# Kernel optimization log

Hardware: AMD Instinct MI355X
Metric: run time of the kernel (lower is better)

The kernel has to match this reference:

```python
import jax, jax.numpy as jnp
import numpy as np

G1 = 8      # channel groups
G2 = 16     # spatial blocks per side
C1, C2 = 128, 64
H1 = W1 = 128
H2 = W2 = 256
BS1 = H1 // G2   # 8  -> 64 elems per x1 block
BS2 = H2 // G2   # 16 -> 256 elems per x2 block
BN_EPS = 1e-5


def setup_inputs() -> dict:
    key = jax.random.key(0)
    ks = jax.random.split(key, 16)
    B = 4
    c1g, c2g = C1 // G1, C2 // G1          # 16, 8
    inp = {
        "x1": jax.random.normal(ks[0], (B, C1, H1, W1), jnp.float32),
        "x2": jax.random.normal(ks[1], (B, C2, H2, W2), jnp.float32),
        # Conv1: conv1d k=1, C1//G1 -> C1//2//G1  (16 -> 8)
        "w_c1": jax.random.normal(ks[2], (c1g // 2, c1g), jnp.float32) * 0.1,
        "b_c1": jnp.zeros((c1g // 2,), jnp.float32),
        # Conv2: conv1d k=1, C2//G1 -> C2//G1  (8 -> 8)
        "w_c2": jax.random.normal(ks[3], (c2g, c2g), jnp.float32) * 0.1,
        "b_c2": jnp.zeros((c2g,), jnp.float32),
        # conv1 / conv2: 1x1 conv2d to 1 channel
        "w_p1": jax.random.normal(ks[4], (C1,), jnp.float32) * 0.1,
        "b_p1": jnp.zeros((), jnp.float32),
        "w_p2": jax.random.normal(ks[5], (C2,), jnp.float32) * 0.1,
        "b_p2": jnp.zeros((), jnp.float32),
        # SpatialAttention linear: 64 -> 256 (torch weight layout [out, in])
        "w_lin": jax.random.normal(ks[6], (BS2 * BS2, BS1 * BS1), jnp.float32) * 0.1,
        "b_lin": jnp.zeros((BS2 * BS2,), jnp.float32),
        # convbnrelu: 1x1 conv C2->C2 + BN (eval mode, running stats mean=0 var=1)
        "w_f": jax.random.normal(ks[7], (C2, C2), jnp.float32) * 0.05,
        "b_f": jnp.zeros((C2,), jnp.float32),
        "bn_gamma": jnp.ones((C2,), jnp.float32),
        "bn_beta": jnp.zeros((C2,), jnp.float32),
    }
    return inp


def reference(x1, x2, w_c1, b_c1, w_c2, b_c2, w_p1, b_p1, w_p2, b_p2,
              w_lin, b_lin, w_f, b_f, bn_gamma, bn_beta):
    B = x1.shape[0]
    c1g, c2g = C1 // G1, C2 // G1

    # ---- grouped channel attention (vectorized over the 8 groups) ----
    gap1 = x1.reshape(B, G1, c1g, H1 * W1).mean(-1)           # [B,g,16]
    gap2 = x2.reshape(B, G1, c2g, H2 * W2).mean(-1)           # [B,g,8]
    mlp1 = jax.nn.relu(jnp.einsum('oc,bgc->bgo', w_c1, gap1) + b_c1)  # [B,g,8]
    mlp2 = jax.nn.relu(jnp.einsum('oc,bgc->bgo', w_c2, gap2) + b_c2)  # [B,g,8]
    sem = jnp.einsum('bgo,bgp->bgop', mlp1, mlp2)             # [B,g,8,8]
    cw_logits = jnp.einsum('bgop,bgp->bgo', sem, mlp2)        # [B,g,8]
    cw = jax.nn.softmax(cw_logits, axis=-1)                   # softmax over channel dim
    sem_x2 = (x2.reshape(B, G1, c2g, H2, W2) * cw[..., None, None]
              ).reshape(B, C2, H2, W2)

    # ---- block-wise spatial attention (vectorized over 16x16 blocks) ----
    nb = G2 * G2
    x1b = x1.reshape(B, C1, G2, BS1, G2, BS1).transpose(0, 2, 4, 1, 3, 5)
    x1b = x1b.reshape(B, nb, C1, BS1, BS1)
    x2b = x2.reshape(B, C2, G2, BS2, G2, BS2).transpose(0, 2, 4, 1, 3, 5)
    x2b = x2b.reshape(B, nb, C2, BS2, BS2)

    pos1 = (jnp.einsum('c,bncij->bnij', w_p1, x1b) + b_p1).reshape(B, nb, BS1 * BS1)
    pos2 = (jnp.einsum('c,bncij->bnij', w_p2, x2b) + b_p2).reshape(B, nb, BS2 * BS2)

    x1t = jnp.einsum('oc,bnc->bno', w_lin, pos1) + b_lin      # [B,nb,256]
    # bmm(x2^T, x1t) is an outer product since both are rank-1 per block
    scores = pos2[..., :, None] * x1t[..., None, :]           # [B,nb,256,256]
    aw = jax.nn.softmax(scores, axis=-1)
    weighted = jnp.einsum('bnq,bnqk->bnk', pos2, aw)          # [B,nb,256]
    # torch.cat(dim=2).view(B,1,H2,W2): raw row-major flatten of block outputs
    spa = weighted.reshape(B, 1, H2, W2)

    # ---- fuse: 1x1 conv + BN(eval) + ReLU ----
    pre = sem_x2 + spa
    conv = jnp.einsum('oc,bchw->bohw', w_f, pre) + b_f[:, None, None]
    bn = conv / jnp.sqrt(jnp.float32(1.0 + BN_EPS)) * bn_gamma[:, None, None] \
         + bn_beta[:, None, None]
    return jax.nn.relu(bn)
```

## Files before the change

### kernel.cpp

```cpp
#include <hip/hip_runtime.h>


#define GAP_OFF  0
#define POS1_OFF 768
#define POS2_OFF 66304

__global__ __launch_bounds__(256) void k_fuse(const float* __restrict__ x1,
                                              const float* __restrict__ x2,
                                              const float* __restrict__ w_p1,
                                              const float* __restrict__ b_p1,
                                              const float* __restrict__ w_p2,
                                              const float* __restrict__ b_p2,
                                              float* __restrict__ ws) {
  __shared__ float gbuf[128 * 65];
  __shared__ float pbuf[1024];
  int blk = blockIdx.x, t = threadIdx.x;
  int wv = t >> 6, ln = t & 63;
  if (blk < 256) {
    int b = blk >> 6;
    int px0 = (blk & 63) << 8;
    const float* xb = x1 + ((size_t)b << 21) + px0 + (ln << 2);
    float4 pacc; pacc.x = pacc.y = pacc.z = pacc.w = 0.f;
    float gs[32];
#pragma unroll
    for (int i = 0; i < 32; ++i) {
      int c = (i << 2) + wv;
      float4 v = *(const float4*)(xb + ((size_t)c << 14));
      float wc = w_p1[c];
      pacc.x = fmaf(wc, v.x, pacc.x); pacc.y = fmaf(wc, v.y, pacc.y);
      pacc.z = fmaf(wc, v.z, pacc.z); pacc.w = fmaf(wc, v.w, pacc.w);
      gs[i] = (v.x + v.y) + (v.z + v.w);
    }
#pragma unroll
    for (int i = 0; i < 32; ++i) gbuf[((wv << 5) + i) * 65 + ln] = gs[i];
    *(float4*)&pbuf[(wv << 8) + (ln << 2)] = pacc;
    __syncthreads();
    if (t < 128) {
      int w2 = t >> 5, i2 = t & 31;
      int c = (i2 << 2) + w2;
      const float* gp = &gbuf[t * 65];
      float s0 = 0.f, s1 = 0.f, s2 = 0.f, s3 = 0.f;
#pragma unroll
      for (int k = 0; k < 64; k += 4) { s0 += gp[k]; s1 += gp[k+1]; s2 += gp[k+2]; s3 += gp[k+3]; }
      atomicAdd(&ws[GAP_OFF + b * 128 + c], (s0 + s1) + (s2 + s3));
    }
    float s = (pbuf[t] + pbuf[256 + t]) + (pbuf[512 + t] + pbuf[768 + t]) + b_p1[0];
    int p = px0 + t, h = p >> 7, w0 = p & 127;
    int n = ((h >> 3) << 4) + (w0 >> 3);
    ws[POS1_OFF + ((b * 256 + n) << 6) + ((h & 7) << 3) + (w0 & 7)] = s;
  } else {
    int j = blk - 256;
    int b = j >> 8;
    int row = j & 255;
    const float* xb = x2 + ((size_t)b << 22) + (row << 8) + (ln << 2);
    float4 pacc; pacc.x = pacc.y = pacc.z = pacc.w = 0.f;
    float gs[16];
#pragma unroll
    for (int i = 0; i < 16; ++i) {
      int c = (i << 2) + wv;
      float4 v = *(const float4*)(xb + ((size_t)c << 16));
      float wc = w_p2[c];
      pacc.x = fmaf(wc, v.x, pacc.x); pacc.y = fmaf(wc, v.y, pacc.y);
      pacc.z = fmaf(wc, v.z, pacc.z); pacc.w = fmaf(wc, v.w, pacc.w);
      gs[i] = (v.x + v.y) + (v.z + v.w);
    }
#pragma unroll
    for (int i = 0; i < 16; ++i) gbuf[((wv << 4) + i) * 65 + ln] = gs[i];
    *(float4*)&pbuf[(wv << 8) + (ln << 2)] = pacc;
    __syncthreads();
    if (t < 64) {
      int w2 = t >> 4, i2 = t & 15;
      int c = (i2 << 2) + w2;
      const float* gp = &gbuf[t * 65];
      float s0 = 0.f, s1 = 0.f, s2 = 0.f, s3 = 0.f;
#pragma unroll
      for (int k = 0; k < 64; k += 4) { s0 += gp[k]; s1 += gp[k+1]; s2 += gp[k+2]; s3 += gp[k+3]; }
      atomicAdd(&ws[GAP_OFF + 512 + b * 64 + c], (s0 + s1) + (s2 + s3));
    }
    float s = (pbuf[t] + pbuf[256 + t]) + (pbuf[512 + t] + pbuf[768 + t]) + b_p2[0];
    int n = ((row >> 4) << 4) + (t >> 4);
    ws[POS2_OFF + ((b * 256 + n) << 8) + ((row & 15) << 4) + (t & 15)] = s;
  }
}

__global__ __launch_bounds__(256) void k_mrg(const float* __restrict__ x2,
                                             const float* __restrict__ w_lin,
                                             const float* __restrict__ b_lin,
                                             const float* __restrict__ w_c1,
                                             const float* __restrict__ b_c1,
                                             const float* __restrict__ w_c2,
                                             const float* __restrict__ b_c2,
                                             const float* __restrict__ w_f,
                                             const float* __restrict__ b_f,
                                             const float* __restrict__ gm,
                                             const float* __restrict__ bt,
                                             const float* __restrict__ ws,
                                             float* __restrict__ out) {
  __shared__ float Mt[4096];
  __shared__ float P1[64], V[256], A2[256], T[256], spa_s[256];
  __shared__ float g1s[128], g2s[64], cw_l[64], p2s[64], p3s[64];
  __shared__ float rmx[4], rmn[4];
  const float L2E = 1.44269504088896f;
  const float kbn = 0.99999500003749969f;
  int t = threadIdx.x;
  int blk = blockIdx.x;
  int b = blk >> 8, n = blk & 255;

  if (t < 128) g1s[t] = ws[GAP_OFF + b * 128 + t] * (1.f / 16384.f);
  if (t < 64)  g2s[t] = ws[GAP_OFF + 512 + b * 64 + t] * (1.f / 65536.f);
  if (t < 64)  P1[t] = ws[POS1_OFF + blk * 64 + t];
  float a = ws[POS2_OFF + blk * 256 + t];
  float a2 = a * L2E;
  A2[t] = a2;
  __syncthreads();

  float v = b_lin[t];
  const float* wr = w_lin + t * 64;
#pragma unroll 16
  for (int c = 0; c < 64; ++c) v = fmaf(wr[c], P1[c], v);
  V[t] = v;
  float vmax = v, vmin = v;
#pragma unroll
  for (int m = 32; m; m >>= 1) {
    vmax = fmaxf(vmax, __shfl_xor(vmax, m));
    vmin = fminf(vmin, __shfl_xor(vmin, m));
  }
  if ((t & 63) == 0) { rmx[t >> 6] = vmax; rmn[t >> 6] = vmin; }
  if (t < 8) {
    int g = t;
    const float* g1 = g1s + g * 16;
    const float* g2 = g2s + g * 8;
    float m1[8];
    for (int o = 0; o < 8; ++o) {
      float s = b_c1[o];
      for (int c = 0; c < 16; ++c) s = fmaf(w_c1[o * 16 + c], g1[c], s);
      m1[o] = fmaxf(s, 0.f);
    }
    float ss = 0.f;
    for (int p = 0; p < 8; ++p) {
      float s = b_c2[p];
      for (int c = 0; c < 8; ++c) s = fmaf(w_c2[p * 8 + c], g2[c], s);
      float r = fmaxf(s, 0.f);
      ss = fmaf(r, r, ss);
    }
    float lg[8], mx = -1e30f;
    for (int o = 0; o < 8; ++o) { lg[o] = m1[o] * ss; mx = fmaxf(mx, lg[o]); }
    float se = 0.f;
    for (int o = 0; o < 8; ++o) {
      lg[o] = __builtin_amdgcn_exp2f((lg[o] - mx) * L2E);
      se += lg[o];
    }
    float inv = 1.f / se;
    for (int o = 0; o < 8; ++o) cw_l[g * 8 + o] = lg[o] * inv;
  }
  __syncthreads();

  vmax = fmaxf(fmaxf(rmx[0], rmx[1]), fmaxf(rmx[2], rmx[3]));
  vmin = fminf(fminf(rmn[0], rmn[1]), fminf(rmn[2], rmn[3]));
  float m2 = (a2 > 0.f) ? a2 * vmax : a2 * vmin;
  float d0 = 0.f, d1 = 0.f, d2 = 0.f, d3 = 0.f;
#pragma unroll 4
  for (int k = 0; k < 256; k += 4) {
    float4 vv = *(float4*)&V[k];
    d0 += __builtin_amdgcn_exp2f(fmaf(a2, vv.x, -m2));
    d1 += __builtin_amdgcn_exp2f(fmaf(a2, vv.y, -m2));
    d2 += __builtin_amdgcn_exp2f(fmaf(a2, vv.z, -m2));
    d3 += __builtin_amdgcn_exp2f(fmaf(a2, vv.w, -m2));
  }
  float den = (d0 + d1) + (d2 + d3);
  T[t] = (a / den) * __builtin_amdgcn_exp2f(-m2);
  if (t < 64) {
    const float4* wrow = (const float4*)(w_f + t * 64);
    float s0 = 0.f, s1 = 0.f, s2 = 0.f, s3 = 0.f;
#pragma unroll
    for (int k = 0; k < 16; ++k) {
      float4 wv = wrow[k];
      s0 += wv.x; s1 += wv.y; s2 += wv.z; s3 += wv.w;
    }
    float A = kbn * gm[t];
    p2s[t] = ((s0 + s1) + (s2 + s3)) * A;
    p3s[t] = fmaf(b_f[t], A, bt[t]);
  }
  __syncthreads();

  float c0 = 0.f, c1 = 0.f, c2 = 0.f, c3 = 0.f;
#pragma unroll 4
  for (int q = 0; q < 256; q += 4) {
    float4 aq = *(float4*)&A2[q];
    float4 tq = *(float4*)&T[q];
    c0 = fmaf(tq.x, __builtin_amdgcn_exp2f(aq.x * v), c0);
    c1 = fmaf(tq.y, __builtin_amdgcn_exp2f(aq.y * v), c1);
    c2 = fmaf(tq.z, __builtin_amdgcn_exp2f(aq.z * v), c2);
    c3 = fmaf(tq.w, __builtin_amdgcn_exp2f(aq.w * v), c3);
  }
  spa_s[t] = (c0 + c1) + (c2 + c3);
#pragma unroll
  for (int i = 0; i < 16; ++i) {
    int idx = i * 256 + t;
    int c = idx >> 6, o = idx & 63;
    Mt[idx] = w_f[o * 64 + c] * cw_l[c] * (kbn * gm[o]);
  }
  __syncthreads();

  int og = (t >> 5) << 3;
  int pA = (t & 31) << 2;
  int pB = pA + 128;
  const float* xg = x2 + ((size_t)b << 22) + (n << 8);
  float acc[8][8];
#pragma unroll
  for (int i = 0; i < 8; ++i)
#pragma unroll
    for (int j = 0; j < 8; ++j) acc[i][j] = 0.f;
#pragma unroll 4
  for (int c = 0; c < 64; ++c) {
    float4 xa = *(const float4*)(xg + ((size_t)c << 16) + pA);
    float4 xb = *(const float4*)(xg + ((size_t)c << 16) + pB);
    float4 ma = *(float4*)&Mt[(c << 6) + og];
    float4 mb = *(float4*)&Mt[(c << 6) + og + 4];
    float xs[8] = {xa.x, xa.y, xa.z, xa.w, xb.x, xb.y, xb.z, xb.w};
    float ms[8] = {ma.x, ma.y, ma.z, ma.w, mb.x, mb.y, mb.z, mb.w};
#pragma unroll
    for (int i = 0; i < 8; ++i)
#pragma unroll
      for (int j = 0; j < 8; ++j)
        acc[i][j] = fmaf(ms[i], xs[j], acc[i][j]);
  }
  float spa[8];
#pragma unroll
  for (int j = 0; j < 4; ++j) { spa[j] = spa_s[pA + j]; spa[4 + j] = spa_s[pB + j]; }
  float* outp = out + ((size_t)b << 22) + (n << 8);
#pragma unroll
  for (int i = 0; i < 8; ++i) {
    int o = og + i;
    float p2 = p2s[o];
    float p3 = p3s[o];
    float r[8];
#pragma unroll
    for (int j = 0; j < 8; ++j)
      r[j] = fmaxf(fmaf(spa[j], p2, acc[i][j] + p3), 0.f);
    float4 r0; r0.x = r[0]; r0.y = r[1]; r0.z = r[2]; r0.w = r[3];
    float4 r1; r1.x = r[4]; r1.y = r[5]; r1.z = r[6]; r1.w = r[7];
    float* po = outp + ((size_t)o << 16);
    *(float4*)(po + pA) = r0;
    *(float4*)(po + pB) = r1;
  }
}

extern "C" void kernel_launch(void* const* d_in, const int* in_sizes, int n_in,
                              void* d_out, int out_size, void* d_ws, size_t ws_size,
                              hipStream_t stream) {
  const float* x1   = (const float*)d_in[0];
  const float* x2   = (const float*)d_in[1];
  const float* w_c1 = (const float*)d_in[2];
  const float* b_c1 = (const float*)d_in[3];
  const float* w_c2 = (const float*)d_in[4];
  const float* b_c2 = (const float*)d_in[5];
  const float* w_p1 = (const float*)d_in[6];
  const float* b_p1 = (const float*)d_in[7];
  const float* w_p2 = (const float*)d_in[8];
  const float* b_p2 = (const float*)d_in[9];
  const float* w_lin= (const float*)d_in[10];
  const float* b_lin= (const float*)d_in[11];
  const float* w_f  = (const float*)d_in[12];
  const float* b_f  = (const float*)d_in[13];
  const float* gmm  = (const float*)d_in[14];
  const float* btt  = (const float*)d_in[15];
  float* ws  = (float*)d_ws;
  float* out = (float*)d_out;

  hipMemsetAsync(ws, 0, 768 * sizeof(float), stream);
  hipLaunchKernelGGL(k_fuse, dim3(1280), dim3(256), 0, stream, x1, x2, w_p1, b_p1, w_p2, b_p2, ws);
  hipLaunchKernelGGL(k_mrg,  dim3(1024), dim3(256), 0, stream, x2, w_lin, b_lin,
                     w_c1, b_c1, w_c2, b_c2, w_f, b_f, gmm, btt, ws, out);
}
```

Baseline: 219.8 us.

## Use bf16 MFMA with split-x for fuse conv; halve k_fuse LDS staging

Replaces the FP32 FMA 64x64 channel-mix in k_mrg with bf16 MFMA 16x16x32. The per-block weight matrix is rounded to bf16 and x2 is split into high and low bf16 parts to keep precision. k_fuse now processes x1 channels in two halves, so its shared reduction buffer is half the size, and k_mrg gains a launch bound for 4 blocks per SM. The weights are kept only at bf16 precision, which adds some error, and the new x2 loads are scalar, strided per lane, instead of float4.

```diff
diff --git a/kernel.cpp b/kernel.cpp
--- a/kernel.cpp
+++ b/kernel.cpp
@@ -4,6 +4,10 @@
 #define GAP_OFF  0
 #define POS1_OFF 768
 #define POS2_OFF 66304
+
+typedef __attribute__((ext_vector_type(8))) short short8;
+typedef __attribute__((ext_vector_type(4))) float f32x4;
+union U8 { short8 s; unsigned int u[4]; };
 
 __global__ __launch_bounds__(256) void k_fuse(const float* __restrict__ x1,
                                               const float* __restrict__ x2,
@@ -12,7 +16,7 @@
                                               const float* __restrict__ w_p2,
                                               const float* __restrict__ b_p2,
                                               float* __restrict__ ws) {
-  __shared__ float gbuf[128 * 65];
+  __shared__ float gbuf[64 * 65];
   __shared__ float pbuf[1024];
   int blk = blockIdx.x, t = threadIdx.x;
   int wv = t >> 6, ln = t & 63;
@@ -21,28 +25,51 @@
     int px0 = (blk & 63) << 8;
     const float* xb = x1 + ((size_t)b << 21) + px0 + (ln << 2);
     float4 pacc; pacc.x = pacc.y = pacc.z = pacc.w = 0.f;
-    float gs[32];
-#pragma unroll
-    for (int i = 0; i < 32; ++i) {
-      int c = (i << 2) + wv;
-      float4 v = *(const float4*)(xb + ((size_t)c << 14));
-      float wc = w_p1[c];
-      pacc.x = fmaf(wc, v.x, pacc.x); pacc.y = fmaf(wc, v.y, pacc.y);
-      pacc.z = fmaf(wc, v.z, pacc.z); pacc.w = fmaf(wc, v.w, pacc.w);
-      gs[i] = (v.x + v.y) + (v.z + v.w);
-    }
-#pragma unroll
-    for (int i = 0; i < 32; ++i) gbuf[((wv << 5) + i) * 65 + ln] = gs[i];
+    {
+      float gs[16];
+#pragma unroll
+      for (int i = 0; i < 16; ++i) {
+        int c = (i << 2) + wv;
+        float4 v = *(const float4*)(xb + ((size_t)c << 14));
+        float wc = w_p1[c];
+        pacc.x = fmaf(wc, v.x, pacc.x); pacc.y = fmaf(wc, v.y, pacc.y);
+        pacc.z = fmaf(wc, v.z, pacc.z); pacc.w = fmaf(wc, v.w, pacc.w);
+        gs[i] = (v.x + v.y) + (v.z + v.w);
+      }
+#pragma unroll
+      for (int i = 0; i < 16; ++i) gbuf[((wv << 4) + i) * 65 + ln] = gs[i];
+    }
+    __syncthreads();
+    if (t < 64) {
+      const float* gp = &gbuf[t * 65];
+      float s0 = 0.f, s1 = 0.f, s2 = 0.f, s3 = 0.f;
+#pragma unroll
+      for (int k = 0; k < 64; k += 4) { s0 += gp[k]; s1 += gp[k+1]; s2 += gp[k+2]; s3 += gp[k+3]; }
+      atomicAdd(&ws[GAP_OFF + b * 128 + ((t & 15) << 2) + (t >> 4)], (s0 + s1) + (s2 + s3));
+    }
+    __syncthreads();
+    {
+      float gs[16];
+#pragma unroll
+      for (int i = 0; i < 16; ++i) {
+        int c = 64 + (i << 2) + wv;
+        float4 v = *(const float4*)(xb + ((size_t)c << 14));
+        float wc = w_p1[c];
+        pacc.x = fmaf(wc, v.x, pacc.x); pacc.y = fmaf(wc, v.y, pacc.y);
+        pacc.z = fmaf(wc, v.z, pacc.z); pacc.w = fmaf(wc, v.w, pacc.w);
+        gs[i] = (v.x + v.y) + (v.z + v.w);
+      }
+#pragma unroll
+      for (int i = 0; i < 16; ++i) gbuf[((wv << 4) + i) * 65 + ln] = gs[i];
+    }
     *(float4*)&pbuf[(wv << 8) + (ln << 2)] = pacc;
     __syncthreads();
-    if (t < 128) {
-      int w2 = t >> 5, i2 = t & 31;
-      int c = (i2 << 2) + w2;
+    if (t < 64) {
       const float* gp = &gbuf[t * 65];
       float s0 = 0.f, s1 = 0.f, s2 = 0.f, s3 = 0.f;
 #pragma unroll
       for (int k = 0; k < 64; k += 4) { s0 += gp[k]; s1 += gp[k+1]; s2 += gp[k+2]; s3 += gp[k+3]; }
-      atomicAdd(&ws[GAP_OFF + b * 128 + c], (s0 + s1) + (s2 + s3));
+      atomicAdd(&ws[GAP_OFF + b * 128 + 64 + ((t & 15) << 2) + (t >> 4)], (s0 + s1) + (s2 + s3));
     }
     float s = (pbuf[t] + pbuf[256 + t]) + (pbuf[512 + t] + pbuf[768 + t]) + b_p1[0];
     int p = px0 + t, h = p >> 7, w0 = p & 127;
@@ -83,20 +110,20 @@
   }
 }
 
-__global__ __launch_bounds__(256) void k_mrg(const float* __restrict__ x2,
-                                             const float* __restrict__ w_lin,
-                                             const float* __restrict__ b_lin,
-                                             const float* __restrict__ w_c1,
-                                             const float* __restrict__ b_c1,
-                                             const float* __restrict__ w_c2,
-                                             const float* __restrict__ b_c2,
-                                             const float* __restrict__ w_f,
-                                             const float* __restrict__ b_f,
-                                             const float* __restrict__ gm,
-                                             const float* __restrict__ bt,
-                                             const float* __restrict__ ws,
-                                             float* __restrict__ out) {
-  __shared__ float Mt[4096];
+__global__ __launch_bounds__(256, 4) void k_mrg(const float* __restrict__ x2,
+                                                const float* __restrict__ w_lin,
+                                                const float* __restrict__ b_lin,
+                                                const float* __restrict__ w_c1,
+                                                const float* __restrict__ b_c1,
+                                                const float* __restrict__ w_c2,
+                                                const float* __restrict__ b_c2,
+                                                const float* __restrict__ w_f,
+                                                const float* __restrict__ b_f,
+                                                const float* __restrict__ gm,
+                                                const float* __restrict__ bt,
+                                                const float* __restrict__ ws,
+                                                float* __restrict__ out) {
+  __shared__ unsigned short aHi[4096];
   __shared__ float P1[64], V[256], A2[256], T[256], spa_s[256];
   __shared__ float g1s[128], g2s[64], cw_l[64], p2s[64], p3s[64];
   __shared__ float rmx[4], rmn[4];
@@ -194,55 +221,91 @@
     c3 = fmaf(tq.w, __builtin_amdgcn_exp2f(aq.w * v), c3);
   }
   spa_s[t] = (c0 + c1) + (c2 + c3);
-#pragma unroll
-  for (int i = 0; i < 16; ++i) {
-    int idx = i * 256 + t;
-    int c = idx >> 6, o = idx & 63;
-    Mt[idx] = w_f[o * 64 + c] * cw_l[c] * (kbn * gm[o]);
+  {
+    unsigned int* aU = (unsigned int*)aHi;
+#pragma unroll
+    for (int gi = 0; gi < 4; ++gi) {
+      int o = (gi << 4) + ((t >> 2) & 15);
+      float ga = kbn * gm[o];
+#pragma unroll
+      for (int gk = 0; gk < 2; ++gk) {
+        int c = (gk << 5) + ((t >> 6) << 3) + ((t & 3) << 1);
+        float2 wf2 = *(const float2*)(w_f + (o << 6) + c);
+        float v0 = wf2.x * cw_l[c] * ga;
+        float v1 = wf2.y * cw_l[c + 1] * ga;
+        unsigned int u0 = __float_as_uint(v0), u1 = __float_as_uint(v1);
+        unsigned int r0 = (u0 + 0x7FFFu + ((u0 >> 16) & 1u)) >> 16;
+        unsigned int r1 = (u1 + 0x7FFFu + ((u1 >> 16) & 1u)) & 0xFFFF0000u;
+        aU[(((gi << 1) + gk) << 8) + t] = r0 | r1;
+      }
+    }
   }
   __syncthreads();
 
-  int og = (t >> 5) << 3;
-  int pA = (t & 31) << 2;
-  int pB = pA + 128;
-  const float* xg = x2 + ((size_t)b << 22) + (n << 8);
-  float acc[8][8];
-#pragma unroll
-  for (int i = 0; i < 8; ++i)
-#pragma unroll
-    for (int j = 0; j < 8; ++j) acc[i][j] = 0.f;
-#pragma unroll 4
-  for (int c = 0; c < 64; ++c) {
-    float4 xa = *(const float4*)(xg + ((size_t)c << 16) + pA);
-    float4 xb = *(const float4*)(xg + ((size_t)c << 16) + pB);
-    float4 ma = *(float4*)&Mt[(c << 6) + og];
-    float4 mb = *(float4*)&Mt[(c << 6) + og + 4];
-    float xs[8] = {xa.x, xa.y, xa.z, xa.w, xb.x, xb.y, xb.z, xb.w};
-    float ms[8] = {ma.x, ma.y, ma.z, ma.w, mb.x, mb.y, mb.z, mb.w};
-#pragma unroll
-    for (int i = 0; i < 8; ++i)
-#pragma unroll
-      for (int j = 0; j < 8; ++j)
-        acc[i][j] = fmaf(ms[i], xs[j], acc[i][j]);
-  }
-  float spa[8];
-#pragma unroll
-  for (int j = 0; j < 4; ++j) { spa[j] = spa_s[pA + j]; spa[4 + j] = spa_s[pB + j]; }
-  float* outp = out + ((size_t)b << 22) + (n << 8);
-#pragma unroll
-  for (int i = 0; i < 8; ++i) {
-    int o = og + i;
-    float p2 = p2s[o];
-    float p3 = p3s[o];
-    float r[8];
-#pragma unroll
-    for (int j = 0; j < 8; ++j)
-      r[j] = fmaxf(fmaf(spa[j], p2, acc[i][j] + p3), 0.f);
-    float4 r0; r0.x = r[0]; r0.y = r[1]; r0.z = r[2]; r0.w = r[3];
-    float4 r1; r1.x = r[4]; r1.y = r[5]; r1.z = r[6]; r1.w = r[7];
-    float* po = outp + ((size_t)o << 16);
-    *(float4*)(po + pA) = r0;
-    *(float4*)(po + pB) = r1;
+  {
+    int l = t & 63;
+    int w = t >> 6;
+    int pcol = l & 15;
+    int krow = l >> 4;
+    short8 afr[4][2];
+#pragma unroll
+    for (int i = 0; i < 4; ++i)
+#pragma unroll
+      for (int ks = 0; ks < 2; ++ks)
+        afr[i][ks] = *(const short8*)&aHi[(((i << 1) + ks) << 9) + (l << 3)];
+    float p2v[16], p3v[16];
+#pragma unroll
+    for (int i = 0; i < 4; ++i)
+#pragma unroll
+      for (int r = 0; r < 4; ++r) {
+        int o = (i << 4) + (krow << 2) + r;
+        p2v[(i << 2) + r] = p2s[o];
+        p3v[(i << 2) + r] = p3s[o];
+      }
+    const float* xbase = x2 + ((size_t)b << 22) + (n << 8) + (w << 6) + pcol
+                         + ((size_t)(krow << 3) << 16);
+    float* obase = out + ((size_t)b << 22) + (n << 8) + (w << 6) + pcol;
+    for (int jt = 0; jt < 4; ++jt) {
+      const float* xp = xbase + (jt << 4);
+      float xv[2][8];
+#pragma unroll
+      for (int ks = 0; ks < 2; ++ks)
+#pragma unroll
+        for (int j = 0; j < 8; ++j)
+          xv[ks][j] = xp[(size_t)((ks << 5) + j) << 16];
+      U8 bh[2], bl[2];
+#pragma unroll
+      for (int ks = 0; ks < 2; ++ks)
+#pragma unroll
+        for (int q = 0; q < 4; ++q) {
+          float f0 = xv[ks][2 * q], f1 = xv[ks][2 * q + 1];
+          unsigned int u0 = __float_as_uint(f0), u1 = __float_as_uint(f1);
+          unsigned int h0 = u0 & 0xFFFF0000u, h1 = u1 & 0xFFFF0000u;
+          bh[ks].u[q] = (u0 >> 16) | h1;
+          float e0 = f0 - __uint_as_float(h0);
+          float e1 = f1 - __uint_as_float(h1);
+          bl[ks].u[q] = (__float_as_uint(e0) >> 16) | (__float_as_uint(e1) & 0xFFFF0000u);
+        }
+      f32x4 acc[4] = {};
+#pragma unroll
+      for (int i = 0; i < 4; ++i) {
+#pragma unroll
+        for (int ks = 0; ks < 2; ++ks) {
+          acc[i] = __builtin_amdgcn_mfma_f32_16x16x32_bf16(afr[i][ks], bh[ks].s, acc[i], 0, 0, 0);
+          acc[i] = __builtin_amdgcn_mfma_f32_16x16x32_bf16(afr[i][ks], bl[ks].s, acc[i], 0, 0, 0);
+        }
+      }
+      float spa_p = spa_s[(w << 6) + (jt << 4) + pcol];
+#pragma unroll
+      for (int i = 0; i < 4; ++i) {
+#pragma unroll
+        for (int r = 0; r < 4; ++r) {
+          int o = (i << 4) + (krow << 2) + r;
+          float val = fmaf(spa_p, p2v[(i << 2) + r], acc[i][r] + p3v[(i << 2) + r]);
+          obase[(jt << 4) + ((size_t)o << 16)] = fmaxf(val, 0.f);
+        }
+      }
+    }
   }
 }
 
```

Result: faster. 199.2 us (-9.4%).
